# Performance work log

Hardware: AMD Instinct MI355X
Metric: run time of the kernel (lower is better)

The kernel has to match this reference:

```python
import jax, jax.numpy as jnp
import numpy as np

B, S, D, E, K = 4, 2048, 1024, 8, 2
H = 4 * D  # expert hidden dim


def setup_inputs() -> dict:
    key = jax.random.key(0)
    ks = jax.random.split(key, 4)
    sc = lambda n: 1.0 / np.sqrt(n)
    return {
        "x": jax.random.normal(ks[0], (B, S, D), jnp.float32),
        "gate_w": jax.random.normal(ks[1], (D, E), jnp.float32) * sc(D),
        "gate_b": jnp.zeros((E,), jnp.float32),
        "w1": jax.random.normal(ks[2], (E, D, H), jnp.float32) * sc(D),
        "b1": jnp.zeros((E, H), jnp.float32),
        "w2": jax.random.normal(ks[3], (E, H, D), jnp.float32) * sc(H),
        "b2": jnp.zeros((E, D), jnp.float32),
    }


def reference(x, gate_w, gate_b, w1, b1, w2, b2):
    Bx, Sx, Dx = x.shape
    n_exp = w1.shape[0]

    # --- TopKRouter: softmax over expert logits, keep top-k scores at their slots ---
    logits = jnp.einsum('bsd,de->bse', x, gate_w) + gate_b          # [B,S,E]
    scores = jax.nn.softmax(logits, axis=-1)
    topk_s, topk_i = jax.lax.top_k(scores, K)                        # [B,S,K]
    onehot = jax.nn.one_hot(topk_i, n_exp, dtype=scores.dtype)       # [B,S,K,E]
    dispatch = jnp.einsum('bske,bsk->bse', onehot, topk_s)           # [B,S,E]

    # --- DynamicMoE combine ---
    xf = x.reshape(-1, Dx)                                           # [B*S, D]
    wf = dispatch.reshape(-1, n_exp)                                 # [B*S, E]
    out = jnp.zeros_like(xf)
    for i in range(n_exp):  # fixed small expert count; sequential overwrite semantics
        wi = wf[:, i:i + 1]                                          # [B*S, 1]
        # routing weight multiplies the expert INPUT (as in the original)
        h = jax.nn.relu((xf * wi) @ w1[i] + b1[i])                   # [B*S, 4D]
        y = h @ w2[i] + b2[i]                                        # [B*S, D]
        # out[mask] = y : later experts overwrite earlier ones
        out = jnp.where(wi > 0, y, out)
    return out.reshape(Bx, Sx, Dx)
```

## Files before the change

### kernel.cpp

```cpp
#include <hip/hip_runtime.h>
#include <hip/hip_bf16.h>
#include <stdint.h>

typedef __attribute__((ext_vector_type(8))) __bf16 bf16x8;
typedef __attribute__((ext_vector_type(4))) __bf16 bf16x4;
typedef __attribute__((ext_vector_type(4))) float  f32x4;

#define NTOK   8192
#define DMODEL 1024
#define HDIM   4096
#define NEXP   8

__device__ __forceinline__ void glds16(const void* g, void* l) {
  __builtin_amdgcn_global_load_lds(
      (const __attribute__((address_space(1))) uint32_t*)g,
      (__attribute__((address_space(3))) uint32_t*)l, 16, 0, 0);
}

#define WAITV(N) asm volatile("s_waitcnt vmcnt(" #N ")" ::: "memory")
#define SBAR()  do { __builtin_amdgcn_sched_barrier(0); \
                     __builtin_amdgcn_s_barrier();      \
                     __builtin_amdgcn_sched_barrier(0); } while (0)

__global__ void zero_cnt_kernel(int* cnt) {
  if (threadIdx.x < NEXP) cnt[threadIdx.x] = 0;
}

__global__ void prefix_kernel(const int* __restrict__ cnt, int* __restrict__ base) {
  if (threadIdx.x == 0) {
    int b = 0;
    base[0] = 0;
    for (int e = 0; e < NEXP; ++e) {
      b += (cnt[e] + 255) & ~255;
      base[e + 1] = b;
    }
  }
}

__device__ void gate_body(int bid,
    const float* __restrict__ x, const float* __restrict__ gw,
    const float* __restrict__ gb, float* __restrict__ wgt,
    int* __restrict__ cnt, int* __restrict__ meta)
{
  const int lane = threadIdx.x & 63;
  const int wv   = threadIdx.x >> 6;
  const int t    = (bid << 2) + wv;
  const float* xp = x + (size_t)t * DMODEL;

  float acc[NEXP];
#pragma unroll
  for (int e = 0; e < NEXP; ++e) acc[e] = 0.f;

#pragma unroll
  for (int j = 0; j < 4; ++j) {
    const int d = j * 256 + lane * 4;
    const float4 xv = *(const float4*)(xp + d);
    const float xs[4] = {xv.x, xv.y, xv.z, xv.w};
#pragma unroll
    for (int dd = 0; dd < 4; ++dd) {
      const float4 g0 = *(const float4*)(gw + (size_t)(d + dd) * NEXP);
      const float4 g1 = *(const float4*)(gw + (size_t)(d + dd) * NEXP + 4);
      acc[0] = fmaf(xs[dd], g0.x, acc[0]);
      acc[1] = fmaf(xs[dd], g0.y, acc[1]);
      acc[2] = fmaf(xs[dd], g0.z, acc[2]);
      acc[3] = fmaf(xs[dd], g0.w, acc[3]);
      acc[4] = fmaf(xs[dd], g1.x, acc[4]);
      acc[5] = fmaf(xs[dd], g1.y, acc[5]);
      acc[6] = fmaf(xs[dd], g1.z, acc[6]);
      acc[7] = fmaf(xs[dd], g1.w, acc[7]);
    }
  }
#pragma unroll
  for (int e = 0; e < NEXP; ++e) {
#pragma unroll
    for (int off = 32; off > 0; off >>= 1)
      acc[e] += __shfl_xor(acc[e], off, 64);
  }
  if (lane == 0) {
    float l[NEXP];
#pragma unroll
    for (int e = 0; e < NEXP; ++e) l[e] = acc[e] + gb[e];
    int i1 = 0; float m1 = l[0];
#pragma unroll
    for (int e = 1; e < NEXP; ++e) if (l[e] > m1) { m1 = l[e]; i1 = e; }
    int i2 = -1; float m2 = -3.402823466e38f;
#pragma unroll
    for (int e = 0; e < NEXP; ++e) if (e != i1 && l[e] > m2) { m2 = l[e]; i2 = e; }
    const int es = i1 > i2 ? i1 : i2;
    float s = 0.f;
#pragma unroll
    for (int e = 0; e < NEXP; ++e) s += expf(l[e] - m1);
    const float w = expf(l[es] - m1) / s;
    wgt[t] = w;
    const int pos = atomicAdd(&cnt[es], 1);
    meta[t] = (es << 13) | pos;
  }
}

template<int N, int K>
__device__ void packw_body(int bid, const float* __restrict__ src,
                           __bf16* __restrict__ dst)
{
  const int NP = N / 128;
  const int np = bid % NP;
  const int e  = (bid / NP) % NEXP;
  const int kt = bid / (NP * NEXP);
  const int t = threadIdx.x;
  __shared__ __bf16 sh[16384];

  const float* sp = src + (size_t)e * K * N + (size_t)(kt * 128) * N + np * 128;
  const int g  = t & 31;
  const int kb = t >> 5;

  float4 vv[16];
#pragma unroll
  for (int i = 0; i < 16; ++i)
    vv[i] = *(const float4*)(sp + (size_t)(kb + 8 * i) * N + g * 4);

#pragma unroll
  for (int i = 0; i < 16; ++i) {
    const int k = kb + 8 * i;
    bf16x4 o;
    o[0] = (__bf16)vv[i].x; o[1] = (__bf16)vv[i].y;
    o[2] = (__bf16)vv[i].z; o[3] = (__bf16)vv[i].w;
    const int pg = (g + 2 * (k >> 3) + (k & 1)) & 31;
    *(bf16x4*)&sh[k * 128 + pg * 4] = o;
  }
  __syncthreads();

  __bf16* dbase = dst + ((size_t)e * N + np * 128) * K + kt * 128;
  const int ks8 = t & 15;
  const int nb  = t >> 4;
#pragma unroll
  for (int i = 0; i < 8; ++i) {
    const int n = nb + 16 * i;
    bf16x8 v;
#pragma unroll
    for (int j = 0; j < 8; ++j) {
      const int k = ks8 * 8 + j;
      const int pg = ((n >> 2) + 2 * (k >> 3) + (k & 1)) & 31;
      v[j] = sh[k * 128 + pg * 4 + (n & 3)];
    }
    *(bf16x8*)(dbase + (size_t)n * K + ks8 * 8) = v;
  }
}

__global__ __launch_bounds__(256) void fusedA_kernel(
    const float* __restrict__ x, const float* __restrict__ gw,
    const float* __restrict__ gb, float* __restrict__ wgt,
    int* __restrict__ cnt, int* __restrict__ meta,
    const float* __restrict__ w1, __bf16* __restrict__ w1p,
    const float* __restrict__ w2, __bf16* __restrict__ w2p)
{
  const int c = blockIdx.x / 3, sel = blockIdx.x % 3;
  if (sel == 0)      gate_body(c, x, gw, gb, wgt, cnt, meta);
  else if (sel == 1) packw_body<HDIM, DMODEL>(c, w1, w1p);
  else               packw_body<DMODEL, HDIM>(c, w2, w2p);
}

__global__ __launch_bounds__(256) void fusedA2_kernel(
    const float* __restrict__ x, const float* __restrict__ gw,
    const float* __restrict__ gb, float* __restrict__ wgt,
    int* __restrict__ cnt, int* __restrict__ meta,
    const float* __restrict__ w1, __bf16* __restrict__ w1p)
{
  const int c = blockIdx.x / 2, sel = blockIdx.x % 2;
  if (sel == 0) gate_body(c, x, gw, gb, wgt, cnt, meta);
  else          packw_body<HDIM, DMODEL>(c, w1, w1p);
}

template<int N, int K>
__global__ __launch_bounds__(256) void pack_w_kernel(
    const float* __restrict__ src, __bf16* __restrict__ dst)
{
  packw_body<N, K>(blockIdx.x, src, dst);
}

__global__ __launch_bounds__(256) void pack_x_kernel(
    const float* __restrict__ x, const float* __restrict__ wgt,
    const int* __restrict__ meta, const int* __restrict__ base,
    __bf16* __restrict__ xbf, int* __restrict__ sortmap)
{
  const int t = blockIdx.x * 2 + (threadIdx.x >> 7);
  const int l = threadIdx.x & 127;
  const int m = meta[t];
  const int es = m >> 13, pos = m & 8191;
  const int dst = base[es] + pos;
  const float w = wgt[t];
  const float4 a = *(const float4*)(x + (size_t)t * DMODEL + l * 8);
  const float4 b = *(const float4*)(x + (size_t)t * DMODEL + l * 8 + 4);
  bf16x8 o;
  o[0] = (__bf16)(a.x * w); o[1] = (__bf16)(a.y * w);
  o[2] = (__bf16)(a.z * w); o[3] = (__bf16)(a.w * w);
  o[4] = (__bf16)(b.x * w); o[5] = (__bf16)(b.y * w);
  o[6] = (__bf16)(b.z * w); o[7] = (__bf16)(b.w * w);
  *(bf16x8*)(xbf + (size_t)dst * DMODEL + l * 8) = o;
  if (l == 0) sortmap[dst] = t;
}

template<int KSTEPS, int ASTRIDE, int NOUT, bool RELU, bool SCATTER, typename OutT>
__global__ __launch_bounds__(512, 1) void moe_gemm256_kernel(
    const __bf16* __restrict__ Am, const __bf16* __restrict__ Bp,
    const float* __restrict__ bias, const int* __restrict__ cnt,
    const int* __restrict__ base, const int* __restrict__ sortmap,
    OutT* __restrict__ outp)
{
  const int e  = blockIdx.z;
  const int ce = cnt[e];
  const int rb = base[e];
  const int cep = base[e + 1] - rb;
  const int m0 = blockIdx.y << 8;
  if (m0 >= cep) return;
  const int np = blockIdx.x, n0 = np << 8;

  const int tid = threadIdx.x, lane = tid & 63, wv = tid >> 6;
  const int wm = wv >> 2, wn = wv & 3;
  const int rl = lane & 15, sl = lane >> 4;

  __shared__ alignas(16) __bf16 lds[65536];

  const __bf16* asrc[4];
  const __bf16* bsrc[4];
#pragma unroll
  for (int i = 0; i < 4; ++i) {
    const int c = (wv * 4 + i) * 64 + lane;
    const int r = c >> 3, p = c & 7;
    const int koff = (p ^ (r & 7)) * 8;
    asrc[i] = Am + (size_t)(rb + m0 + r) * ASTRIDE + koff;
    bsrc[i] = Bp + ((size_t)(e * (NOUT / 128) + np * 2) * 128 + r) * ASTRIDE + koff;
  }

  auto stage = [&](int buf, int ks) {
    __bf16* Ad = lds + buf * 32768;
    __bf16* Bd = Ad + 16384;
#pragma unroll
    for (int i = 0; i < 4; ++i)
      glds16(asrc[i] + ks * 64, Ad + (wv * 4 + i) * 512);
#pragma unroll
    for (int i = 0; i < 4; ++i)
      glds16(bsrc[i] + ks * 64, Bd + (wv * 4 + i) * 512);
  };

  f32x4 acc[8][4] = {};

  stage(0, 0);
  for (int ks = 0; ks < KSTEPS; ++ks) {
    const int buf = ks & 1;
    WAITV(0);
    SBAR();
    if (ks + 1 < KSTEPS) stage(buf ^ 1, ks + 1);

    const char* Ab = (const char*)lds + buf * 65536 + wm * 16384;
    const char* Bb = (const char*)lds + buf * 65536 + 32768 + (wn >> 1) * 16384;

#pragma unroll
    for (int kk = 0; kk < 2; ++kk) {
      bf16x8 af[8];
#pragma unroll
      for (int mf = 0; mf < 8; ++mf) {
        const int row = mf * 16 + rl;
        af[mf] = *(const bf16x8*)(Ab + row * 128 + (((kk * 4 + sl) ^ (row & 7)) << 4));
      }
#pragma unroll
      for (int nh = 0; nh < 2; ++nh) {
        bf16x8 bf2[2];
#pragma unroll
        for (int nf2 = 0; nf2 < 2; ++nf2) {
          const int row = (wn & 1) * 64 + nh * 32 + nf2 * 16 + rl;
          bf2[nf2] = *(const bf16x8*)(Bb + row * 128 + (((kk * 4 + sl) ^ (row & 7)) << 4));
        }
        __builtin_amdgcn_s_setprio(1);
#pragma unroll
        for (int mf = 0; mf < 8; ++mf)
#pragma unroll
          for (int nf2 = 0; nf2 < 2; ++nf2)
            acc[mf][nh * 2 + nf2] = __builtin_amdgcn_mfma_f32_16x16x32_bf16(
                af[mf], bf2[nf2], acc[mf][nh * 2 + nf2], 0, 0, 0);
        __builtin_amdgcn_s_setprio(0);
      }
    }
  }

  float bb[4];
#pragma unroll
  for (int nf = 0; nf < 4; ++nf)
    bb[nf] = bias[(size_t)e * NOUT + n0 + wn * 64 + nf * 16 + rl];

#pragma unroll
  for (int mf = 0; mf < 8; ++mf) {
#pragma unroll
    for (int j = 0; j < 4; ++j) {
      const int gm = m0 + wm * 128 + mf * 16 + sl * 4 + j;
      if constexpr (SCATTER) {
        if (gm < ce) {
          const int tok = sortmap[rb + gm];
          OutT* op = outp + (size_t)tok * NOUT + n0 + wn * 64;
#pragma unroll
          for (int nf = 0; nf < 4; ++nf)
            op[nf * 16 + rl] = (OutT)(acc[mf][nf][j] + bb[nf]);
        }
      } else {
        OutT* op = outp + (size_t)(rb + gm) * NOUT + n0 + wn * 64;
        const bool live = gm < ce;
#pragma unroll
        for (int nf = 0; nf < 4; ++nf) {
          float v = acc[mf][nf][j] + bb[nf];
          if constexpr (RELU) v = fmaxf(v, 0.f);
          op[nf * 16 + rl] = live ? (OutT)v : (OutT)0.f;
        }
      }
    }
  }
}

extern "C" void kernel_launch(void* const* d_in, const int* in_sizes, int n_in,
                              void* d_out, int out_size, void* d_ws, size_t ws_size,
                              hipStream_t stream)
{
  const float* x  = (const float*)d_in[0];
  const float* gw = (const float*)d_in[1];
  const float* gb = (const float*)d_in[2];
  const float* w1 = (const float*)d_in[3];
  const float* b1 = (const float*)d_in[4];
  const float* w2 = (const float*)d_in[5];
  const float* b2 = (const float*)d_in[6];
  float* out = (float*)d_out;

  char* ws = (char*)d_ws;
  int*    cnt     = (int*)ws;
  int*    base    = (int*)(ws + 256);
  int*    meta    = (int*)(ws + 4096);
  float*  wgt     = (float*)(ws + 40960);
  int*    sortmap = (int*)(ws + 81920);
  __bf16* xbf     = (__bf16*)(ws + ((size_t)1   << 20));
  __bf16* hmat    = (__bf16*)(ws + ((size_t)22  << 20));
  __bf16* w1p     = (__bf16*)(ws + ((size_t)106 << 20));

  const bool conc = ws_size >= ((size_t)235 << 20);

  zero_cnt_kernel<<<1, 64, 0, stream>>>(cnt);

  if (conc) {
    __bf16* w2p = (__bf16*)(ws + ((size_t)170 << 20));
    fusedA_kernel<<<6144, 256, 0, stream>>>(
        x, gw, gb, wgt, cnt, meta, w1, w1p, w2, w2p);
    prefix_kernel<<<1, 64, 0, stream>>>(cnt, base);
    pack_x_kernel<<<NTOK / 2, 256, 0, stream>>>(x, wgt, meta, base, xbf, sortmap);
    moe_gemm256_kernel<DMODEL / 64, DMODEL, HDIM, true, false, __bf16>
        <<<dim3(HDIM / 256, 40, NEXP), 512, 0, stream>>>(
            xbf, w1p, b1, cnt, base, sortmap, hmat);
    moe_gemm256_kernel<HDIM / 64, HDIM, DMODEL, false, true, float>
        <<<dim3(DMODEL / 256, 40, NEXP), 512, 0, stream>>>(
            hmat, w2p, b2, cnt, base, sortmap, out);
  } else {
    fusedA2_kernel<<<4096, 256, 0, stream>>>(
        x, gw, gb, wgt, cnt, meta, w1, w1p);
    prefix_kernel<<<1, 64, 0, stream>>>(cnt, base);
    pack_x_kernel<<<NTOK / 2, 256, 0, stream>>>(x, wgt, meta, base, xbf, sortmap);
    moe_gemm256_kernel<DMODEL / 64, DMODEL, HDIM, true, false, __bf16>
        <<<dim3(HDIM / 256, 40, NEXP), 512, 0, stream>>>(
            xbf, w1p, b1, cnt, base, sortmap, hmat);
    pack_w_kernel<DMODEL, HDIM><<<2048, 256, 0, stream>>>(w2, w1p);
    moe_gemm256_kernel<HDIM / 64, HDIM, DMODEL, false, true, float>
        <<<dim3(DMODEL / 256, 40, NEXP), 512, 0, stream>>>(
            hmat, w1p, b2, cnt, base, sortmap, out);
  }
}
```

Before: 341.7 us.

## Split-K the second expert GEMM four ways with a bf16 partial combine kernel

The down-projection GEMM (K=4096, N=1024) ran only 4 N-tiles per expert, which gave too few workgroups to fill the GPU. It is now split four ways along K, so each block writes bf16 partial sums into reused workspace buffers (the w1p and xbf regions). A new combine kernel then sums the four partials, adds the bias, and scatters rows to token order. This raises parallelism and shortens each block's K loop. In exchange it adds partial-buffer traffic, an extra launch, and bf16 rounding of the partials.

```diff
diff --git a/kernel.cpp b/kernel.cpp
--- a/kernel.cpp
+++ b/kernel.cpp
@@ -10,6 +10,7 @@
 #define DMODEL 1024
 #define HDIM   4096
 #define NEXP   8
+#define PSTRIDE 10240
 
 __device__ __forceinline__ void glds16(const void* g, void* l) {
   __builtin_amdgcn_global_load_lds(
@@ -198,20 +199,26 @@
   if (l == 0) sortmap[dst] = t;
 }
 
-template<int KSTEPS, int ASTRIDE, int NOUT, bool RELU, bool SCATTER, typename OutT>
+template<int KSTEPS, int SPLITK, int ASTRIDE, int NOUT, bool RELU,
+         bool SCATTER, bool ADDBIAS, typename OutT>
 __global__ __launch_bounds__(512, 1) void moe_gemm256_kernel(
     const __bf16* __restrict__ Am, const __bf16* __restrict__ Bp,
     const float* __restrict__ bias, const int* __restrict__ cnt,
     const int* __restrict__ base, const int* __restrict__ sortmap,
-    OutT* __restrict__ outp)
+    OutT* __restrict__ outp, OutT* __restrict__ outp2)
 {
   const int e  = blockIdx.z;
   const int ce = cnt[e];
   const int rb = base[e];
   const int cep = base[e + 1] - rb;
-  const int m0 = blockIdx.y << 8;
+  const int m  = blockIdx.y % 40;
+  const int kh = (SPLITK > 1) ? (blockIdx.y / 40) : 0;
+  const int m0 = m << 8;
   if (m0 >= cep) return;
   const int np = blockIdx.x, n0 = np << 8;
+
+  constexpr int KH = KSTEPS / SPLITK;
+  const int kbase = kh * KH * 64;
 
   const int tid = threadIdx.x, lane = tid & 63, wv = tid >> 6;
   const int wm = wv >> 2, wn = wv & 3;
@@ -225,7 +232,7 @@
   for (int i = 0; i < 4; ++i) {
     const int c = (wv * 4 + i) * 64 + lane;
     const int r = c >> 3, p = c & 7;
-    const int koff = (p ^ (r & 7)) * 8;
+    const int koff = (p ^ (r & 7)) * 8 + kbase;
     asrc[i] = Am + (size_t)(rb + m0 + r) * ASTRIDE + koff;
     bsrc[i] = Bp + ((size_t)(e * (NOUT / 128) + np * 2) * 128 + r) * ASTRIDE + koff;
   }
@@ -244,11 +251,11 @@
   f32x4 acc[8][4] = {};
 
   stage(0, 0);
-  for (int ks = 0; ks < KSTEPS; ++ks) {
+  for (int ks = 0; ks < KH; ++ks) {
     const int buf = ks & 1;
     WAITV(0);
     SBAR();
-    if (ks + 1 < KSTEPS) stage(buf ^ 1, ks + 1);
+    if (ks + 1 < KH) stage(buf ^ 1, ks + 1);
 
     const char* Ab = (const char*)lds + buf * 65536 + wm * 16384;
     const char* Bb = (const char*)lds + buf * 65536 + 32768 + (wn >> 1) * 16384;
@@ -281,10 +288,17 @@
     }
   }
 
-  float bb[4];
-#pragma unroll
-  for (int nf = 0; nf < 4; ++nf)
-    bb[nf] = bias[(size_t)e * NOUT + n0 + wn * 64 + nf * 16 + rl];
+  float bb[4] = {0.f, 0.f, 0.f, 0.f};
+  if constexpr (ADDBIAS) {
+#pragma unroll
+    for (int nf = 0; nf < 4; ++nf)
+      bb[nf] = bias[(size_t)e * NOUT + n0 + wn * 64 + nf * 16 + rl];
+  }
+
+  OutT* obase = outp;
+  if constexpr (SPLITK > 1)
+    obase = (kh == SPLITK - 1) ? outp2
+                               : outp + (size_t)kh * ((size_t)PSTRIDE * NOUT);
 
 #pragma unroll
   for (int mf = 0; mf < 8; ++mf) {
@@ -294,13 +308,13 @@
       if constexpr (SCATTER) {
         if (gm < ce) {
           const int tok = sortmap[rb + gm];
-          OutT* op = outp + (size_t)tok * NOUT + n0 + wn * 64;
+          OutT* op = obase + (size_t)tok * NOUT + n0 + wn * 64;
 #pragma unroll
           for (int nf = 0; nf < 4; ++nf)
             op[nf * 16 + rl] = (OutT)(acc[mf][nf][j] + bb[nf]);
         }
       } else {
-        OutT* op = outp + (size_t)(rb + gm) * NOUT + n0 + wn * 64;
+        OutT* op = obase + (size_t)(rb + gm) * NOUT + n0 + wn * 64;
         const bool live = gm < ce;
 #pragma unroll
         for (int nf = 0; nf < 4; ++nf) {
@@ -311,6 +325,34 @@
       }
     }
   }
+}
+
+__global__ __launch_bounds__(256) void combine_kernel(
+    const __bf16* __restrict__ p0, const __bf16* __restrict__ p3,
+    const float* __restrict__ b2, const int* __restrict__ cnt,
+    const int* __restrict__ base, const int* __restrict__ sortmap,
+    float* __restrict__ out)
+{
+  const int r = blockIdx.x;
+  int e = 0;
+#pragma unroll
+  for (int ee = 0; ee < NEXP; ++ee) if (r >= base[ee + 1]) e = ee + 1;
+  if (e >= NEXP || (r - base[e]) >= cnt[e]) return;
+  const int tok = sortmap[r];
+  const int n = threadIdx.x * 4;
+  const size_t off = (size_t)r * DMODEL + n;
+  const size_t stride = (size_t)PSTRIDE * DMODEL;
+  float a0 = 0.f, a1 = 0.f, a2 = 0.f, a3 = 0.f;
+#pragma unroll
+  for (int kh = 0; kh < 4; ++kh) {
+    const __bf16* p = (kh == 3) ? (p3 + off) : (p0 + kh * stride + off);
+    const bf16x4 v = *(const bf16x4*)p;
+    a0 += (float)v[0]; a1 += (float)v[1];
+    a2 += (float)v[2]; a3 += (float)v[3];
+  }
+  const float4 bbv = *(const float4*)(b2 + (size_t)e * DMODEL + n);
+  float4 o = {a0 + bbv.x, a1 + bbv.y, a2 + bbv.z, a3 + bbv.w};
+  *(float4*)(out + (size_t)tok * DMODEL + n) = o;
 }
 
 extern "C" void kernel_launch(void* const* d_in, const int* in_sizes, int n_in,
@@ -342,27 +384,32 @@
 
   if (conc) {
     __bf16* w2p = (__bf16*)(ws + ((size_t)170 << 20));
+    __bf16* part0 = w1p;
+    __bf16* part3 = xbf;
+
     fusedA_kernel<<<6144, 256, 0, stream>>>(
         x, gw, gb, wgt, cnt, meta, w1, w1p, w2, w2p);
     prefix_kernel<<<1, 64, 0, stream>>>(cnt, base);
     pack_x_kernel<<<NTOK / 2, 256, 0, stream>>>(x, wgt, meta, base, xbf, sortmap);
-    moe_gemm256_kernel<DMODEL / 64, DMODEL, HDIM, true, false, __bf16>
+    moe_gemm256_kernel<DMODEL / 64, 1, DMODEL, HDIM, true, false, true, __bf16>
         <<<dim3(HDIM / 256, 40, NEXP), 512, 0, stream>>>(
-            xbf, w1p, b1, cnt, base, sortmap, hmat);
-    moe_gemm256_kernel<HDIM / 64, HDIM, DMODEL, false, true, float>
-        <<<dim3(DMODEL / 256, 40, NEXP), 512, 0, stream>>>(
-            hmat, w2p, b2, cnt, base, sortmap, out);
+            xbf, w1p, b1, cnt, base, sortmap, hmat, hmat);
+    moe_gemm256_kernel<HDIM / 64, 4, HDIM, DMODEL, false, false, false, __bf16>
+        <<<dim3(DMODEL / 256, 4 * 40, NEXP), 512, 0, stream>>>(
+            hmat, w2p, b2, cnt, base, sortmap, part0, part3);
+    combine_kernel<<<PSTRIDE, 256, 0, stream>>>(
+        part0, part3, b2, cnt, base, sortmap, out);
   } else {
     fusedA2_kernel<<<4096, 256, 0, stream>>>(
         x, gw, gb, wgt, cnt, meta, w1, w1p);
     prefix_kernel<<<1, 64, 0, stream>>>(cnt, base);
     pack_x_kernel<<<NTOK / 2, 256, 0, stream>>>(x, wgt, meta, base, xbf, sortmap);
-    moe_gemm256_kernel<DMODEL / 64, DMODEL, HDIM, true, false, __bf16>
+    moe_gemm256_kernel<DMODEL / 64, 1, DMODEL, HDIM, true, false, true, __bf16>
         <<<dim3(HDIM / 256, 40, NEXP), 512, 0, stream>>>(
-            xbf, w1p, b1, cnt, base, sortmap, hmat);
+            xbf, w1p, b1, cnt, base, sortmap, hmat, hmat);
     pack_w_kernel<DMODEL, HDIM><<<2048, 256, 0, stream>>>(w2, w1p);
-    moe_gemm256_kernel<HDIM / 64, HDIM, DMODEL, false, true, float>
+    moe_gemm256_kernel<HDIM / 64, 1, HDIM, DMODEL, false, true, true, float>
         <<<dim3(DMODEL / 256, 40, NEXP), 512, 0, stream>>>(
-            hmat, w1p, b2, cnt, base, sortmap, out);
-  }
-}
+            hmat, w1p, b2, cnt, base, sortmap, out, out);
+  }
+}
```

Result: slower. 361.4 us (+5.8%).
